# Performance work log

Hardware: AMD Instinct MI355X
Metric: run time of the kernel (lower is better)

The kernel has to match this reference:

```python
import jax, jax.numpy as jnp
import numpy as np

NUM_INPUTS = 2048
NUM_GATES = 8192
BATCH = 2048


def setup_inputs() -> dict:
    key = jax.random.key(0)
    k1, k2, k3 = jax.random.split(key, 3)
    x = jax.random.uniform(k1, (BATCH, NUM_INPUTS), dtype=jnp.float32)
    w = jax.random.normal(k2, (16, NUM_GATES), dtype=jnp.float32)
    c = jax.random.normal(k3, (NUM_INPUTS, NUM_GATES, 2), dtype=jnp.float32)
    return {"x": x, "w": w, "c": c}


def reference(x, w, c):
    num_inputs, num_gates, _ = c.shape
    # softmax over input wires -> soft connection matrix [I, 2G]
    connections = jax.nn.softmax(c, axis=0).reshape(num_inputs, num_gates * 2)
    y = (x @ connections).reshape(x.shape[0], num_gates, 2)  # [B, G, 2]
    A = y[:, :, 0]  # [B, G]
    B = y[:, :, 1]  # [B, G]
    AB = A * B
    ones = jnp.ones_like(A)
    zeros = jnp.zeros_like(A)
    g7 = A + B - AB
    g6 = g7 - AB
    # 16 soft logic gates, stacked on a leading axis: [16, B, G]
    gates = jnp.stack([
        zeros, AB, A - AB, A, B - AB, B, g6, g7,
        ones - g7, ones - g6, ones - B, ones - (B - AB),
        ones - A, ones - (A - AB), ones - AB, ones,
    ], axis=0)
    weights = jax.nn.softmax(w, axis=0)  # [16, G]
    # weighted combine over gate types -> [B, G]
    out = jnp.einsum('kbg,kg->bg', gates, weights)
    return out
```

## Files before the change

kernel.cpp:

```cpp
#include <hip/hip_runtime.h>
#include <hip/hip_bf16.h>
#include <stdint.h>

#define BATCH   2048
#define NIN     2048
#define NGATES  8192
#define NCOL    16384

typedef short s16x8 __attribute__((ext_vector_type(8)));
typedef float f32x4 __attribute__((ext_vector_type(4)));

__device__ __forceinline__ void gload_lds16(const void* g, void* l) {
  __builtin_amdgcn_global_load_lds(
      (const __attribute__((address_space(1))) void*)g,
      (__attribute__((address_space(3))) void*)l,
      16, 0, 0);
}

__device__ __forceinline__ unsigned short f2bf(float f) {
  __hip_bfloat16 h = __float2bfloat16(f);
  return __builtin_bit_cast(unsigned short, h);
}
__device__ __forceinline__ float bf2f(unsigned int u) {
  return __bfloat162float(__builtin_bit_cast(__hip_bfloat16,
                                             (unsigned short)(u & 0xffff)));
}

__global__ __launch_bounds__(256) void pre_k(const float4* __restrict__ x,
                                             ushort4* __restrict__ xb,
                                             const float* __restrict__ w,
                                             float4* __restrict__ coeff) {
  const int b = blockIdx.x;
  const int t = threadIdx.x;
  if (b < 4096) {
    const int i = b * 256 + t;
    float4 v = x[i];
    ushort4 h;
    h.x = f2bf(v.x); h.y = f2bf(v.y); h.z = f2bf(v.z); h.w = f2bf(v.w);
    xb[i] = h;
  } else {
    const int g = (b - 4096) * 256 + t;
    float e[16];
    float s = 0.f;
#pragma unroll
    for (int k = 0; k < 16; ++k) { e[k] = __expf(w[k * NGATES + g]); s += e[k]; }
    const float inv = 1.0f / s;
#pragma unroll
    for (int k = 0; k < 16; ++k) e[k] *= inv;
    const float P0 = e[8] + e[9] + e[10] + e[11] + e[12] + e[13] + e[14] + e[15];
    const float P1 = e[2] + e[3] + e[6] + e[7] - e[8] - e[9] - e[12] - e[13];
    const float P2 = e[4] + e[5] + e[6] + e[7] - e[8] - e[9] - e[10] - e[11];
    const float P3 = e[1] - e[2] - e[4] - 2.f * e[6] - e[7] + e[8] + 2.f * e[9]
                   + e[11] + e[13] - e[14];
    coeff[g] = make_float4(P0, P1, P2, P3);
  }
}

__global__ __launch_bounds__(256) void softmax_t_k(const float* __restrict__ c,
                                                   unsigned short* __restrict__ bT,
                                                   float* __restrict__ psums) {
  extern __shared__ char sm3[];
  char*  tile = sm3;
  float* red  = (float*)(sm3 + 65536);
  const int t = threadIdx.x;
  const int ng = (t & 15) * 4;
  const int kg = t >> 4;
  const int n0 = blockIdx.x * 64;
  const int q  = blockIdx.y;
  const float* cb = c + (size_t)n0 + ng;
  float s0 = 0.f, s1 = 0.f, s2 = 0.f, s3 = 0.f;

  float4 v[8], nv[8];
  {
    const int r0 = q * 512 + kg * 8;
#pragma unroll
    for (int d = 0; d < 8; ++d)
      v[d] = *(const float4*)&cb[(size_t)(r0 + d) * NCOL];
  }
  for (int it = 0; it < 4; ++it) {
    if (it < 3) {
      const int r1 = q * 512 + (it + 1) * 128 + kg * 8;
#pragma unroll
      for (int d = 0; d < 8; ++d)
        nv[d] = *(const float4*)&cb[(size_t)(r1 + d) * NCOL];
    }
    unsigned int u[4][4];
#pragma unroll
    for (int d2 = 0; d2 < 4; ++d2) {
      float4 e0 = v[2 * d2], e1 = v[2 * d2 + 1];
      unsigned int a0 = f2bf(__expf(e0.x)), b0 = f2bf(__expf(e1.x));
      unsigned int a1 = f2bf(__expf(e0.y)), b1 = f2bf(__expf(e1.y));
      unsigned int a2 = f2bf(__expf(e0.z)), b2 = f2bf(__expf(e1.z));
      unsigned int a3 = f2bf(__expf(e0.w)), b3 = f2bf(__expf(e1.w));
      s0 += bf2f(a0) + bf2f(b0);
      s1 += bf2f(a1) + bf2f(b1);
      s2 += bf2f(a2) + bf2f(b2);
      s3 += bf2f(a3) + bf2f(b3);
      u[0][d2] = a0 | (b0 << 16);
      u[1][d2] = a1 | (b1 << 16);
      u[2][d2] = a2 | (b2 << 16);
      u[3][d2] = a3 | (b3 << 16);
    }
    const int chunk = it * 16 + kg;
#pragma unroll
    for (int j = 0; j < 4; ++j) {
      const int row = ng + j;
      const int sw  = (chunk & ~7) | ((chunk ^ (row >> 2)) & 7);
      uint4 pk = make_uint4(u[j][0], u[j][1], u[j][2], u[j][3]);
      *(uint4*)&tile[row * 1024 + sw * 16] = pk;
    }
    if (it < 3) {
#pragma unroll
      for (int d = 0; d < 8; ++d) v[d] = nv[d];
    }
  }
  red[kg * 68 + ng + 0] = s0;
  red[kg * 68 + ng + 1] = s1;
  red[kg * 68 + ng + 2] = s2;
  red[kg * 68 + ng + 3] = s3;
  __syncthreads();

  {
    const int wv = t >> 6;
    const int l  = t & 63;
#pragma unroll
    for (int r16 = 0; r16 < 16; ++r16) {
      const int row = wv * 16 + r16;
      const int sw  = (l & ~7) | ((l ^ (row >> 2)) & 7);
      uint4 vv = *(const uint4*)&tile[row * 1024 + sw * 16];
      *(uint4*)&bT[(size_t)(n0 + row) * NIN + q * 512 + l * 8] = vv;
    }
  }
  if (t < 64) {
    float tot = 0.f;
#pragma unroll
    for (int k2 = 0; k2 < 16; ++k2) tot += red[k2 * 68 + t];
    psums[(size_t)q * NCOL + n0 + t] = tot;
  }
}

#define MFMA_B16(a, b, c) __builtin_amdgcn_mfma_f32_16x16x32_bf16(a, b, c, 0, 0, 0)

__global__ __launch_bounds__(512, 2) void gemm_gate_k(
    const unsigned short* __restrict__ xb,
    const unsigned short* __restrict__ bT,
    const float* __restrict__ ps,
    const float4* __restrict__ coeff,
    float* __restrict__ out) {
  extern __shared__ char smem[];
  constexpr int NT = 32;

  const int t  = threadIdx.x;
  const int l  = t & 63;
  const int w  = t >> 6;
  const int wm = w >> 2;
  const int wn = w & 3;
  const int fr = l & 15;
  const int cq = l >> 4;

  const int bid = blockIdx.x;
  const int xcd = bid & 7;
  const int loc = bid >> 3;
  const int m0  = (loc & 7) * 256;
  const int g0  = (xcd * 8 + (loc >> 3)) * 128;

  uint32_t offA[2][2], offB[2][2];
#pragma unroll
  for (int r = 0; r < 2; ++r) {
    const int idx = r * 512 + t;
    const int lr  = idx >> 3;
    const int ch  = (idx & 7) ^ (lr & 7);
    const int rA  = (lr & 63) + ((lr >> 6) << 7);
    offA[0][r] = (uint32_t)(m0 + rA) * NIN + ch * 8;
    offA[1][r] = offA[0][r] + (uint32_t)64 * NIN;
    offB[0][r] = (uint32_t)(2 * (g0 + lr)) * NIN + ch * 8;
    offB[1][r] = offB[0][r] + NIN;
  }

  auto issueA = [&](int u, int tt) {
    char* d = smem + ((tt & 1) << 16) + (u << 14) + t * 16;
    gload_lds16(xb + offA[u][0] + tt * 64, d);
    gload_lds16(xb + offA[u][1] + tt * 64, d + 8192);
  };
  auto issueB = [&](int u, int tt) {
    char* d = smem + ((tt & 1) << 16) + ((2 + u) << 14) + t * 16;
    gload_lds16(bT + offB[u][0] + tt * 64, d);
    gload_lds16(bT + offB[u][1] + tt * 64, d + 8192);
  };

  const int aob = (wm * 64 + fr) * 128;
  const int bob = 32768 + (wn * 32 + fr) * 128;
  const int sx0 = ((cq)     ^ (fr & 7)) * 16;
  const int sx1 = ((cq + 4) ^ (fr & 7)) * 16;

  f32x4 acc[8][4] = {};
  s16x8 af[8];
  s16x8 bfr[8];

  issueA(0, 0); issueA(1, 0); issueB(0, 0); issueB(1, 0);
  issueA(0, 1); issueB(0, 1); issueB(1, 1);
  asm volatile("s_waitcnt vmcnt(6)" ::: "memory");
  asm volatile("s_barrier" ::: "memory");

  for (int kt = 0; kt < NT; ++kt) {
    char* rb = smem + ((kt & 1) << 16);

#pragma unroll
    for (int i = 0; i < 4; ++i) {
      af[i * 2 + 0] = *(const s16x8*)(rb + aob + i * 2048 + sx0);
      af[i * 2 + 1] = *(const s16x8*)(rb + aob + i * 2048 + sx1);
    }
#pragma unroll
    for (int j = 0; j < 2; ++j) {
      bfr[j * 2 + 0] = *(const s16x8*)(rb + bob + j * 2048 + sx0);
      bfr[j * 2 + 1] = *(const s16x8*)(rb + bob + j * 2048 + sx1);
    }
    if (kt + 1 < NT) issueA(1, kt + 1);
    asm volatile("s_barrier" ::: "memory");
    asm volatile("s_waitcnt lgkmcnt(0)" ::: "memory");
    __builtin_amdgcn_s_setprio(1);
#pragma unroll
    for (int i = 0; i < 4; ++i)
#pragma unroll
      for (int j = 0; j < 2; ++j) {
        acc[i][j] = MFMA_B16(af[i * 2 + 0], bfr[j * 2 + 0], acc[i][j]);
        acc[i][j] = MFMA_B16(af[i * 2 + 1], bfr[j * 2 + 1], acc[i][j]);
      }
    __builtin_amdgcn_s_setprio(0);
    asm volatile("s_barrier" ::: "memory");

#pragma unroll
    for (int j = 0; j < 2; ++j) {
      bfr[4 + j * 2 + 0] = *(const s16x8*)(rb + bob + 16384 + j * 2048 + sx0);
      bfr[4 + j * 2 + 1] = *(const s16x8*)(rb + bob + 16384 + j * 2048 + sx1);
    }
    if (kt + 2 < NT) issueA(0, kt + 2);
    asm volatile("s_barrier" ::: "memory");
    asm volatile("s_waitcnt lgkmcnt(0)" ::: "memory");
    __builtin_amdgcn_s_setprio(1);
#pragma unroll
    for (int i = 0; i < 4; ++i)
#pragma unroll
      for (int j = 0; j < 2; ++j) {
        acc[i][2 + j] = MFMA_B16(af[i * 2 + 0], bfr[4 + j * 2 + 0], acc[i][2 + j]);
        acc[i][2 + j] = MFMA_B16(af[i * 2 + 1], bfr[4 + j * 2 + 1], acc[i][2 + j]);
      }
    __builtin_amdgcn_s_setprio(0);
    asm volatile("s_barrier" ::: "memory");

#pragma unroll
    for (int i = 0; i < 4; ++i) {
      af[i * 2 + 0] = *(const s16x8*)(rb + 16384 + aob + i * 2048 + sx0);
      af[i * 2 + 1] = *(const s16x8*)(rb + 16384 + aob + i * 2048 + sx1);
    }
    if (kt + 2 < NT) issueB(0, kt + 2);
    asm volatile("s_barrier" ::: "memory");
    asm volatile("s_waitcnt lgkmcnt(0)" ::: "memory");
    __builtin_amdgcn_s_setprio(1);
#pragma unroll
    for (int i = 0; i < 4; ++i)
#pragma unroll
      for (int j = 0; j < 2; ++j) {
        acc[4 + i][2 + j] = MFMA_B16(af[i * 2 + 0], bfr[4 + j * 2 + 0], acc[4 + i][2 + j]);
        acc[4 + i][2 + j] = MFMA_B16(af[i * 2 + 1], bfr[4 + j * 2 + 1], acc[4 + i][2 + j]);
      }
    __builtin_amdgcn_s_setprio(0);
    asm volatile("s_barrier" ::: "memory");

    if (kt + 2 < NT) issueB(1, kt + 2);
    asm volatile("s_barrier" ::: "memory");
    asm volatile("s_waitcnt lgkmcnt(0)" ::: "memory");
    __builtin_amdgcn_s_setprio(1);
#pragma unroll
    for (int i = 0; i < 4; ++i)
#pragma unroll
      for (int j = 0; j < 2; ++j) {
        acc[4 + i][j] = MFMA_B16(af[i * 2 + 0], bfr[j * 2 + 0], acc[4 + i][j]);
        acc[4 + i][j] = MFMA_B16(af[i * 2 + 1], bfr[j * 2 + 1], acc[4 + i][j]);
      }
    __builtin_amdgcn_s_setprio(0);
    if (kt < NT - 2) {
      asm volatile("s_waitcnt vmcnt(6)" ::: "memory");
    } else {
      asm volatile("s_waitcnt vmcnt(0)" ::: "memory");
    }
    asm volatile("s_barrier" ::: "memory");
  }

#pragma unroll
  for (int j = 0; j < 2; ++j) {
    const int gate = g0 + wn * 32 + j * 16 + fr;
    const int nA = 2 * gate, nB = 2 * gate + 1;
    const float sA = ps[nA] + ps[NCOL + nA] + ps[2 * NCOL + nA] + ps[3 * NCOL + nA];
    const float sB = ps[nB] + ps[NCOL + nB] + ps[2 * NCOL + nB] + ps[3 * NCOL + nB];
    const float ivA = 1.0f / sA;
    const float ivB = 1.0f / sB;
    const float4 P = coeff[gate];
#pragma unroll
    for (int i = 0; i < 8; ++i) {
#pragma unroll
      for (int r = 0; r < 4; ++r) {
        const float A = acc[i][j][r]     * ivA;
        const float B = acc[i][j + 2][r] * ivB;
        const float res = P.x + P.y * A + P.z * B + P.w * A * B;
        const int m = m0 + wm * 128 + i * 16 + cq * 4 + r;
        out[(size_t)m * NGATES + gate] = res;
      }
    }
  }
}

extern "C" void kernel_launch(void* const* d_in, const int* in_sizes, int n_in,
                              void* d_out, int out_size, void* d_ws,
                              size_t ws_size, hipStream_t stream) {
  const float* x = (const float*)d_in[0];
  const float* w = (const float*)d_in[1];
  const float* c = (const float*)d_in[2];
  float* out = (float*)d_out;
  char* ws = (char*)d_ws;

  unsigned short* xb = (unsigned short*)(ws);
  unsigned short* bT = (unsigned short*)(ws + 8388608);
  float4*         cf = (float4*)(ws + 75563008);
  float*          psv = (float*)(ws + 75694080);

  static bool attr_done = false;
  if (!attr_done) {
    (void)hipFuncSetAttribute(reinterpret_cast<const void*>(gemm_gate_k),
                              hipFuncAttributeMaxDynamicSharedMemorySize,
                              131072);
    (void)hipFuncSetAttribute(reinterpret_cast<const void*>(softmax_t_k),
                              hipFuncAttributeMaxDynamicSharedMemorySize,
                              69888);
    attr_done = true;
  }

  pre_k<<<4128, 256, 0, stream>>>((const float4*)x, (ushort4*)xb, w, cf);
  dim3 sg(NCOL / 64, 4);
  softmax_t_k<<<sg, 256, 69888, stream>>>(c, bT, psv);
  gemm_gate_k<<<512, 512, 131072, stream>>>(xb, bT, psv, cf, out);
}
```

Baseline: 347.2 us.

## Halve GEMM grid with two gate tiles per block and split softmax over eight K-chunks

The GEMM kernel now launches 256 persistent-ish blocks, each processing two consecutive 128-gate tiles in one continuous 64-step pipeline, with the epilogue run mid-loop and accumulators reset. The softmax/transpose kernel splits K into 8 chunks of 256 rows instead of 4 of 512, which halves its LDS footprint and doubles its grid for more occupancy. The aim is to avoid pipeline drain/refill between tiles and a partial wave in the GEMM, and to raise parallelism in the softmax stage. The cost is a longer per-block critical path, an epilogue inside the loop, and more partial sums to reduce.

```diff
diff --git a/kernel.cpp b/kernel.cpp
--- a/kernel.cpp
+++ b/kernel.cpp
@@ -61,7 +61,7 @@
                                                    float* __restrict__ psums) {
   extern __shared__ char sm3[];
   char*  tile = sm3;
-  float* red  = (float*)(sm3 + 65536);
+  float* red  = (float*)(sm3 + 32768);
   const int t = threadIdx.x;
   const int ng = (t & 15) * 4;
   const int kg = t >> 4;
@@ -72,14 +72,14 @@
 
   float4 v[8], nv[8];
   {
-    const int r0 = q * 512 + kg * 8;
+    const int r0 = q * 256 + kg * 8;
 #pragma unroll
     for (int d = 0; d < 8; ++d)
       v[d] = *(const float4*)&cb[(size_t)(r0 + d) * NCOL];
   }
-  for (int it = 0; it < 4; ++it) {
-    if (it < 3) {
-      const int r1 = q * 512 + (it + 1) * 128 + kg * 8;
+  for (int it = 0; it < 2; ++it) {
+    if (it < 1) {
+      const int r1 = q * 256 + 128 + kg * 8;
 #pragma unroll
       for (int d = 0; d < 8; ++d)
         nv[d] = *(const float4*)&cb[(size_t)(r1 + d) * NCOL];
@@ -107,9 +107,9 @@
       const int row = ng + j;
       const int sw  = (chunk & ~7) | ((chunk ^ (row >> 2)) & 7);
       uint4 pk = make_uint4(u[j][0], u[j][1], u[j][2], u[j][3]);
-      *(uint4*)&tile[row * 1024 + sw * 16] = pk;
-    }
-    if (it < 3) {
+      *(uint4*)&tile[row * 512 + sw * 16] = pk;
+    }
+    if (it < 1) {
 #pragma unroll
       for (int d = 0; d < 8; ++d) v[d] = nv[d];
     }
@@ -124,11 +124,12 @@
     const int wv = t >> 6;
     const int l  = t & 63;
 #pragma unroll
-    for (int r16 = 0; r16 < 16; ++r16) {
-      const int row = wv * 16 + r16;
-      const int sw  = (l & ~7) | ((l ^ (row >> 2)) & 7);
-      uint4 vv = *(const uint4*)&tile[row * 1024 + sw * 16];
-      *(uint4*)&bT[(size_t)(n0 + row) * NIN + q * 512 + l * 8] = vv;
+    for (int r8 = 0; r8 < 8; ++r8) {
+      const int row = wv * 16 + r8 * 2 + (l >> 5);
+      const int ch  = l & 31;
+      const int sw  = (ch & ~7) | ((ch ^ (row >> 2)) & 7);
+      uint4 vv = *(const uint4*)&tile[row * 512 + sw * 16];
+      *(uint4*)&bT[(size_t)(n0 + row) * NIN + q * 256 + ch * 8] = vv;
     }
   }
   if (t < 64) {
@@ -148,7 +149,7 @@
     const float4* __restrict__ coeff,
     float* __restrict__ out) {
   extern __shared__ char smem[];
-  constexpr int NT = 32;
+  constexpr int NVT = 64;
 
   const int t  = threadIdx.x;
   const int l  = t & 63;
@@ -162,7 +163,7 @@
   const int xcd = bid & 7;
   const int loc = bid >> 3;
   const int m0  = (loc & 7) * 256;
-  const int g0  = (xcd * 8 + (loc >> 3)) * 128;
+  const int g0  = (xcd * 8 + (loc >> 3) * 2) * 128;
 
   uint32_t offA[2][2], offB[2][2];
 #pragma unroll
@@ -177,15 +178,18 @@
     offB[1][r] = offB[0][r] + NIN;
   }
 
-  auto issueA = [&](int u, int tt) {
-    char* d = smem + ((tt & 1) << 16) + (u << 14) + t * 16;
-    gload_lds16(xb + offA[u][0] + tt * 64, d);
-    gload_lds16(xb + offA[u][1] + tt * 64, d + 8192);
+  auto issueA = [&](int u, int tta) {
+    const uint32_t kb = (uint32_t)(tta & 31) * 64;
+    char* d = smem + ((tta & 1) << 16) + (u << 14) + t * 16;
+    gload_lds16(xb + offA[u][0] + kb, d);
+    gload_lds16(xb + offA[u][1] + kb, d + 8192);
   };
-  auto issueB = [&](int u, int tt) {
-    char* d = smem + ((tt & 1) << 16) + ((2 + u) << 14) + t * 16;
-    gload_lds16(bT + offB[u][0] + tt * 64, d);
-    gload_lds16(bT + offB[u][1] + tt * 64, d + 8192);
+  auto issueB = [&](int u, int tta) {
+    const uint32_t kb = (uint32_t)(tta & 31) * 64;
+    const uint32_t pb = (uint32_t)(tta >> 5) * (256u * NIN);
+    char* d = smem + ((tta & 1) << 16) + ((2 + u) << 14) + t * 16;
+    gload_lds16(bT + offB[u][0] + pb + kb, d);
+    gload_lds16(bT + offB[u][1] + pb + kb, d + 8192);
   };
 
   const int aob = (wm * 64 + fr) * 128;
@@ -197,13 +201,41 @@
   s16x8 af[8];
   s16x8 bfr[8];
 
+  auto epilogue = [&](int gp) {
+#pragma unroll
+    for (int j = 0; j < 2; ++j) {
+      const int gate = gp + wn * 32 + j * 16 + fr;
+      const int nA = 2 * gate, nB = 2 * gate + 1;
+      float sA = 0.f, sB = 0.f;
+#pragma unroll
+      for (int qq = 0; qq < 8; ++qq) {
+        sA += ps[qq * NCOL + nA];
+        sB += ps[qq * NCOL + nB];
+      }
+      const float ivA = 1.0f / sA;
+      const float ivB = 1.0f / sB;
+      const float4 P = coeff[gate];
+#pragma unroll
+      for (int i = 0; i < 8; ++i) {
+#pragma unroll
+        for (int r = 0; r < 4; ++r) {
+          const float A = acc[i][j][r]     * ivA;
+          const float B = acc[i][j + 2][r] * ivB;
+          const float res = P.x + P.y * A + P.z * B + P.w * A * B;
+          const int m = m0 + wm * 128 + i * 16 + cq * 4 + r;
+          out[(size_t)m * NGATES + gate] = res;
+        }
+      }
+    }
+  };
+
   issueA(0, 0); issueA(1, 0); issueB(0, 0); issueB(1, 0);
   issueA(0, 1); issueB(0, 1); issueB(1, 1);
   asm volatile("s_waitcnt vmcnt(6)" ::: "memory");
   asm volatile("s_barrier" ::: "memory");
 
-  for (int kt = 0; kt < NT; ++kt) {
-    char* rb = smem + ((kt & 1) << 16);
+  for (int tt = 0; tt < NVT; ++tt) {
+    char* rb = smem + ((tt & 1) << 16);
 
 #pragma unroll
     for (int i = 0; i < 4; ++i) {
@@ -215,7 +247,8 @@
       bfr[j * 2 + 0] = *(const s16x8*)(rb + bob + j * 2048 + sx0);
       bfr[j * 2 + 1] = *(const s16x8*)(rb + bob + j * 2048 + sx1);
     }
-    if (kt + 1 < NT) issueA(1, kt + 1);
+    if (tt + 1 < NVT) issueA(1, tt + 1);
+    asm volatile("s_waitcnt lgkmcnt(8)" ::: "memory");
     asm volatile("s_barrier" ::: "memory");
     asm volatile("s_waitcnt lgkmcnt(0)" ::: "memory");
     __builtin_amdgcn_s_setprio(1);
@@ -234,7 +267,7 @@
       bfr[4 + j * 2 + 0] = *(const s16x8*)(rb + bob + 16384 + j * 2048 + sx0);
       bfr[4 + j * 2 + 1] = *(const s16x8*)(rb + bob + 16384 + j * 2048 + sx1);
     }
-    if (kt + 2 < NT) issueA(0, kt + 2);
+    if (tt + 2 < NVT) issueA(0, tt + 2);
     asm volatile("s_barrier" ::: "memory");
     asm volatile("s_waitcnt lgkmcnt(0)" ::: "memory");
     __builtin_amdgcn_s_setprio(1);
@@ -253,7 +286,7 @@
       af[i * 2 + 0] = *(const s16x8*)(rb + 16384 + aob + i * 2048 + sx0);
       af[i * 2 + 1] = *(const s16x8*)(rb + 16384 + aob + i * 2048 + sx1);
     }
-    if (kt + 2 < NT) issueB(0, kt + 2);
+    if (tt + 2 < NVT) issueB(0, tt + 2);
     asm volatile("s_barrier" ::: "memory");
     asm volatile("s_waitcnt lgkmcnt(0)" ::: "memory");
     __builtin_amdgcn_s_setprio(1);
@@ -267,7 +300,7 @@
     __builtin_amdgcn_s_setprio(0);
     asm volatile("s_barrier" ::: "memory");
 
-    if (kt + 2 < NT) issueB(1, kt + 2);
+    if (tt + 2 < NVT) issueB(1, tt + 2);
     asm volatile("s_barrier" ::: "memory");
     asm volatile("s_waitcnt lgkmcnt(0)" ::: "memory");
     __builtin_amdgcn_s_setprio(1);
@@ -279,35 +312,23 @@
         acc[4 + i][j] = MFMA_B16(af[i * 2 + 1], bfr[j * 2 + 1], acc[4 + i][j]);
       }
     __builtin_amdgcn_s_setprio(0);
-    if (kt < NT - 2) {
+    if (tt < NVT - 2) {
       asm volatile("s_waitcnt vmcnt(6)" ::: "memory");
     } else {
       asm volatile("s_waitcnt vmcnt(0)" ::: "memory");
     }
     asm volatile("s_barrier" ::: "memory");
-  }
-
-#pragma unroll
-  for (int j = 0; j < 2; ++j) {
-    const int gate = g0 + wn * 32 + j * 16 + fr;
-    const int nA = 2 * gate, nB = 2 * gate + 1;
-    const float sA = ps[nA] + ps[NCOL + nA] + ps[2 * NCOL + nA] + ps[3 * NCOL + nA];
-    const float sB = ps[nB] + ps[NCOL + nB] + ps[2 * NCOL + nB] + ps[3 * NCOL + nB];
-    const float ivA = 1.0f / sA;
-    const float ivB = 1.0f / sB;
-    const float4 P = coeff[gate];
-#pragma unroll
-    for (int i = 0; i < 8; ++i) {
-#pragma unroll
-      for (int r = 0; r < 4; ++r) {
-        const float A = acc[i][j][r]     * ivA;
-        const float B = acc[i][j + 2][r] * ivB;
-        const float res = P.x + P.y * A + P.z * B + P.w * A * B;
-        const int m = m0 + wm * 128 + i * 16 + cq * 4 + r;
-        out[(size_t)m * NGATES + gate] = res;
-      }
-    }
-  }
+
+    if (tt == 31) {
+      epilogue(g0);
+#pragma unroll
+      for (int i = 0; i < 8; ++i)
+#pragma unroll
+        for (int j = 0; j < 4; ++j) acc[i][j] = (f32x4){0.f, 0.f, 0.f, 0.f};
+    }
+  }
+
+  epilogue(g0 + 128);
 }
 
 extern "C" void kernel_launch(void* const* d_in, const int* in_sizes, int n_in,
@@ -321,8 +342,8 @@
 
   unsigned short* xb = (unsigned short*)(ws);
   unsigned short* bT = (unsigned short*)(ws + 8388608);
-  float4*         cf = (float4*)(ws + 75563008);
-  float*          psv = (float*)(ws + 75694080);
+  float*          psv = (float*)(ws + 75497472);
+  float4*         cf = (float4*)(ws + 76021760);
 
   static bool attr_done = false;
   if (!attr_done) {
@@ -331,12 +352,12 @@
                               131072);
     (void)hipFuncSetAttribute(reinterpret_cast<const void*>(softmax_t_k),
                               hipFuncAttributeMaxDynamicSharedMemorySize,
-                              69888);
+                              37120);
     attr_done = true;
   }
 
   pre_k<<<4128, 256, 0, stream>>>((const float4*)x, (ushort4*)xb, w, cf);
-  dim3 sg(NCOL / 64, 4);
-  softmax_t_k<<<sg, 256, 69888, stream>>>(c, bT, psv);
-  gemm_gate_k<<<512, 512, 131072, stream>>>(xb, bT, psv, cf, out);
-}
+  dim3 sg(NCOL / 64, 8);
+  softmax_t_k<<<sg, 256, 37120, stream>>>(c, bT, psv);
+  gemm_gate_k<<<256, 512, 131072, stream>>>(xb, bT, psv, cf, out);
+}
```

New measurement: 391.9 us. +12.9%, slower.
